# Performance work log

Hardware: AMD Instinct MI355X
Metric: run time of the kernel (lower is better)

Reference implementation:

```python
import jax, jax.numpy as jnp
import numpy as np
import math

NUM_CONVS = 4
GN_GROUPS = 32
GN_EPS = 1e-5
FPN_STRIDES = (8, 16, 32, 64, 128)
PRIOR_PROB = 0.01


def conv3x3(x, w, b):
    # x: [N,C,H,W], w: [O,I,3,3]
    y = jax.lax.conv_general_dilated(
        x, w, window_strides=(1, 1), padding='SAME',
        dimension_numbers=('NCHW', 'OIHW', 'NCHW'))
    return y + b[None, :, None, None]


def group_norm(x, gamma, beta):
    n, c, h, w = x.shape
    xg = x.reshape(n, GN_GROUPS, c // GN_GROUPS, h, w)
    mean = xg.mean(axis=(2, 3, 4), keepdims=True)
    var = xg.var(axis=(2, 3, 4), keepdims=True)
    xn = ((xg - mean) * jax.lax.rsqrt(var + GN_EPS)).reshape(n, c, h, w)
    return xn * gamma[None, :, None, None] + beta[None, :, None, None]


def subnet(x, ws, bs, gws, gbs):
    # NUM_CONVS x (conv3x3 -> GN -> ReLU)
    for i in range(NUM_CONVS):
        x = jax.nn.relu(group_norm(conv3x3(x, ws[i], bs[i]), gws[i], gbs[i]))
    return x


def permute_to_N_HWA_K(x, k):
    n = x.shape[0]
    return x.transpose(0, 2, 3, 1).reshape(n, -1, k)


def setup_inputs() -> dict:
    key = jax.random.key(0)
    ks = jax.random.split(key, 16)
    C, K = 256, 80
    feats = {
        'p3': jax.random.normal(ks[0], (1, C, 80, 80), jnp.float32),
        'p4': jax.random.normal(ks[1], (1, C, 40, 40), jnp.float32),
        'p5': jax.random.normal(ks[2], (1, C, 20, 20), jnp.float32),
        'p6': jax.random.normal(ks[3], (1, C, 10, 10), jnp.float32),
        'p7': jax.random.normal(ks[4], (1, C, 5, 5), jnp.float32),
    }
    std = 0.01
    bias_value = -math.log((1 - PRIOR_PROB) / PRIOR_PROB)
    params = {
        'cls_w': std * jax.random.normal(ks[5], (NUM_CONVS, C, C, 3, 3), jnp.float32),
        'cls_b': jnp.zeros((NUM_CONVS, C), jnp.float32),
        'cls_gn_w': jnp.ones((NUM_CONVS, C), jnp.float32),
        'cls_gn_b': jnp.zeros((NUM_CONVS, C), jnp.float32),
        'box_w': std * jax.random.normal(ks[6], (NUM_CONVS, C, C, 3, 3), jnp.float32),
        'box_b': jnp.zeros((NUM_CONVS, C), jnp.float32),
        'box_gn_w': jnp.ones((NUM_CONVS, C), jnp.float32),
        'box_gn_b': jnp.zeros((NUM_CONVS, C), jnp.float32),
        'score_w': std * jax.random.normal(ks[7], (K, C, 3, 3), jnp.float32),
        'score_b': jnp.full((K,), bias_value, jnp.float32),
        'pred_w': std * jax.random.normal(ks[8], (4, C, 3, 3), jnp.float32),
        'pred_b': jnp.zeros((4,), jnp.float32),
        'iou_w': std * jax.random.normal(ks[9], (1, C, 3, 3), jnp.float32),
        'iou_b': jnp.zeros((1,), jnp.float32),
        'scales': jnp.ones((5,), jnp.float32),
    }
    return {**feats, **params}


def reference(p3, p4, p5, p6, p7,
              cls_w, cls_b, cls_gn_w, cls_gn_b,
              box_w, box_b, box_gn_w, box_gn_b,
              score_w, score_b, pred_w, pred_b, iou_w, iou_b, scales):
    features = [p3, p4, p5, p6, p7]
    logits, bbox_reg, ious = [], [], []
    for l, feat in enumerate(features):
        c = subnet(feat, cls_w, cls_b, cls_gn_w, cls_gn_b)
        b = subnet(feat, box_w, box_b, box_gn_w, box_gn_b)
        logit = conv3x3(c, score_w, score_b)          # [N,80,H,W]
        iou = conv3x3(b, iou_w, iou_b)                # [N,1,H,W]
        bp = conv3x3(b, pred_w, pred_b) * scales[l]   # Scale module
        # norm_reg_targets=True branch
        reg = jax.nn.relu(bp) * FPN_STRIDES[l]        # [N,4,H,W]
        logits.append(permute_to_N_HWA_K(logit, 80))
        bbox_reg.append(permute_to_N_HWA_K(reg, 4))
        ious.append(permute_to_N_HWA_K(iou, 1))
    box_cls = jnp.concatenate(logits, axis=1)    # [N, sumHW, 80]
    box_delta = jnp.concatenate(bbox_reg, axis=1)  # [N, sumHW, 4]
    box_iou = jnp.concatenate(ious, axis=1)      # [N, sumHW, 1]
    # pack into one array for a single output: [N, sumHW, 85]
    return jnp.concatenate([box_cls, box_delta, box_iou], axis=-1)
```

## Files before the change

### kernel.cpp

```cpp
#include <hip/hip_runtime.h>

typedef unsigned short u16;
typedef __attribute__((ext_vector_type(8))) short bf16x8;
typedef __attribute__((ext_vector_type(4))) float f32x4;

#define NLEV 5
#define CCH 256
#define KTOT 2304
#define P_TOT 8525
#define PP_TOT 9165
#define PLS (PP_TOT*64)
#define HSTR 11776

__constant__ int   c_HW[NLEV]     = {6400, 1600, 400, 100, 25};
__constant__ int   c_W[NLEV]      = {80, 40, 20, 10, 5};
__constant__ int   c_off[NLEV]    = {0, 6400, 8000, 8400, 8500};
__constant__ int   c_poff[NLEV]   = {0, 6724, 8488, 8972, 9116};
__constant__ int   c_tls[NLEV+1]  = {0, 50, 65, 71, 73, 74};
__constant__ int   c_ntx[NLEV]    = {5, 3, 2, 1, 1};
__constant__ float c_stridef[NLEV]= {8.f, 16.f, 32.f, 64.f, 128.f};

__device__ __forceinline__ u16 f2bf(float f){
  union { float f; unsigned u; } v; v.f = f;
  unsigned r = v.u + 0x7fffu + ((v.u >> 16) & 1u);
  return (u16)(r >> 16);
}

__device__ __forceinline__ void g2l16(const u16* g, u16* l, int lane){
#if defined(__has_builtin)
#if __has_builtin(__builtin_amdgcn_global_load_lds)
  __builtin_amdgcn_global_load_lds(
      (const __attribute__((address_space(1))) unsigned int*)g,
      (__attribute__((address_space(3))) unsigned int*)l, 16, 0, 0);
  return;
#endif
#endif
  *(uint4*)(l + lane*8) = *(const uint4*)g;
}

#define WAIT_VM4   0x0F74
#define WAIT_VM10  0x0F7A
#define WAIT_VM0   0x0F70
#define WAIT_LGKM0 0xC07F

template<int MODE>
__global__ __launch_bounds__(256, 2) void gemm_conv(
    const u16* __restrict__ Xc, const u16* __restrict__ Xb,
    const u16* __restrict__ Wc, const u16* __restrict__ Wb,
    const float* __restrict__ bc, const float* __restrict__ bb,
    float* __restrict__ Yc, float* __restrict__ Yb,
    float* __restrict__ stats,
    const float* __restrict__ predb, const float* __restrict__ ioub,
    const float* __restrict__ scales, float* __restrict__ out)
{
  __shared__ u16 hB[2*HSTR];
  __shared__ u16 sA[4][2][2048];
  __shared__ float sstat[16][2];

  const int ptile = blockIdx.x;
  const int mtile = (MODE == 0) ? blockIdx.y : 0;
  const int br = blockIdx.z;
  int lv = 0;
  #pragma unroll
  for (int i = 1; i < NLEV; i++) if (ptile >= c_tls[i]) lv = i;
  const int tidx = ptile - c_tls[lv];
  const int ntx = c_ntx[lv];
  const int ty0 = (tidx / ntx) * 8, tx0 = (tidx - (tidx / ntx) * ntx) * 16;
  const int W = c_W[lv], wrow2 = W + 2;

  const int tid = threadIdx.x, wv = tid >> 6, ln = tid & 63;
  const int quad = ln >> 4, l15 = ln & 15;

  const u16* __restrict__ X  = br ? Xb : Xc;
  const u16* __restrict__ WA = br ? Wb : Wc;

  const int ASTR = (MODE == 0) ? 16384 : 8192;
  const u16* abase = WA +
      (size_t)(((MODE == 0) ? mtile*16 : 0) + wv*4) * 512 + ln*8;

  const u16* hptr[6]; int hslab[6];
  #pragma unroll
  for (int i = 0; i < 6; i++) {
    int j = wv + 4*i;
    if (j > 22) j -= 4;
    hslab[i] = j;
    const int item = j*64 + ln;
    int hp = item >> 3; if (hp >= 180) hp -= 180;
    const int g = item & 7;
    const int hy = hp / 18, hx = hp - hy*18;
    const int prow = c_poff[lv] + (ty0 + hy)*wrow2 + tx0 + hx;
    hptr[i] = X + (size_t)prow*64 + ((g ^ (hp & 7)) << 3);
  }

  auto stageH = [&](int plane) {
    u16* dst = &hB[(plane & 1) * HSTR];
    const size_t cof = (size_t)plane * PLS;
    #pragma unroll
    for (int i = 0; i < 6; i++)
      g2l16(hptr[i] + cof, dst + hslab[i]*512, ln);
  };
  auto stageA = [&](int s, int b) {
    const u16* as = abase + (size_t)s * ASTR;
    u16* da = &sA[wv][b][0];
    #pragma unroll
    for (int j = 0; j < 4; j++) g2l16(as + j*512, da + j*512, ln);
  };

  f32x4 acc[2][8];
  #pragma unroll
  for (int i = 0; i < 2; i++)
    #pragma unroll
    for (int j = 0; j < 8; j++) acc[i][j] = (f32x4){0.f, 0.f, 0.f, 0.f};

  if (MODE == 0 && tid < 32) sstat[tid >> 1][tid & 1] = 0.f;

  stageH(0);
  stageH(1);
  stageA(0, 0);
  stageA(4, 1);
  __syncthreads();

  int cc = 0, tap = 0;
  #pragma unroll 1
  for (int t = 0; t < 36; t++) {
    if (t == 10 || t == 19) __builtin_amdgcn_s_waitcnt(WAIT_VM10);
    else if (t == 35)       __builtin_amdgcn_s_waitcnt(WAIT_VM0);
    else                    __builtin_amdgcn_s_waitcnt(WAIT_VM4);
    if (tap == 0 && cc > 0) {
      __builtin_amdgcn_sched_barrier(0);
      __builtin_amdgcn_s_barrier();
      __builtin_amdgcn_sched_barrier(0);
      if (cc < 3) stageH(cc + 1);
    }
    const u16* myA = &sA[wv][t & 1][0];
    const u16* hpl = &hB[(cc & 1) * HSTR];
    const int dh = tap / 3, dw = tap - dh*3;
    bf16x8 af[2][2], bf[2][8];
    #pragma unroll
    for (int sub = 0; sub < 2; sub++) {
      const int q = sub*4 + quad;
      const int swzA = (q ^ (l15 & 7)) * 8;
      #pragma unroll
      for (int mt = 0; mt < 2; mt++)
        af[sub][mt] = *(const bf16x8*)&myA[(mt*16 + l15)*64 + swzA];
      #pragma unroll
      for (int nt = 0; nt < 8; nt++) {
        const int hp = (nt + dh)*18 + l15 + dw;
        bf[sub][nt] = *(const bf16x8*)&hpl[hp*64 + ((q ^ (hp & 7)) << 3)];
      }
    }
    __builtin_amdgcn_s_waitcnt(WAIT_LGKM0);
    if (t < 34) {
      int tap2 = tap + 2, cc2 = cc;
      if (tap2 >= 9) { tap2 -= 9; cc2++; }
      stageA(tap2*4 + cc2, t & 1);
    }
    #pragma unroll
    for (int sub = 0; sub < 2; sub++)
      #pragma unroll
      for (int mt = 0; mt < 2; mt++)
        #pragma unroll
        for (int nt = 0; nt < 8; nt++)
          acc[mt][nt] = __builtin_amdgcn_mfma_f32_16x16x32_bf16(
              af[sub][mt], bf[sub][nt], acc[mt][nt], 0, 0, 0);
    if (++tap == 9) { tap = 0; cc++; }
  }

  const int gx = tx0 + l15;
  if (MODE == 0) {
    const float* __restrict__ bias = br ? bb : bc;
    float* __restrict__ Y = br ? Yb : Yc;
    #pragma unroll
    for (int mt = 0; mt < 2; mt++) {
      const int mloc = wv*32 + mt*16 + quad*4;
      const int mrow = mtile*128 + mloc;
      const f32x4 bv = *(const f32x4*)&bias[mrow];
      float s = 0.f, sq = 0.f;
      #pragma unroll
      for (int nt = 0; nt < 8; nt++) {
        const int gy = ty0 + nt;
        f32x4 v = acc[mt][nt] + bv;
        if (gy < W && gx < W) {
          const size_t n = (size_t)(c_off[lv] + gy*W + gx);
          *(f32x4*)&Y[n*CCH + mrow] = v;
          #pragma unroll
          for (int r = 0; r < 4; r++) { s += v[r]; sq += v[r]*v[r]; }
        }
      }
      #pragma unroll
      for (int o = 1; o < 16; o <<= 1) { s += __shfl_xor(s, o); sq += __shfl_xor(sq, o); }
      if (l15 == 0) {
        const int g = mloc >> 3;
        atomicAdd(&sstat[g][0], s);
        atomicAdd(&sstat[g][1], sq);
      }
    }
    __syncthreads();
    if (tid < 32) {
      const int g = tid >> 1, c = tid & 1;
      atomicAdd(&stats[((br*NLEV + lv)*32 + mtile*16 + g)*2 + c], sstat[g][c]);
    }
  } else {
    const float scl = scales[lv];
    const float stf = c_stridef[lv];
    #pragma unroll
    for (int mt = 0; mt < 2; mt++) {
      const int mr0 = wv*32 + mt*16 + quad*4;
      if (mr0 >= 85) continue;
      #pragma unroll
      for (int nt = 0; nt < 8; nt++) {
        const int gy = ty0 + nt;
        if (gy >= W || gx >= W) continue;
        const size_t n = (size_t)(c_off[lv] + gy*W + gx);
        const f32x4 v = acc[mt][nt];
        #pragma unroll
        for (int r = 0; r < 4; r++) {
          const int m = mr0 + r;
          if (br == 0) {
            if (m < 80) out[n*85 + m] = v[r] + bc[m];
          } else {
            if (m < 4) {
              const float t = (v[r] + predb[m]) * scl;
              out[n*85 + 80 + m] = fmaxf(t, 0.f) * stf;
            } else if (m == 4) {
              out[n*85 + 84] = v[r] + ioub[0];
            }
          }
        }
      }
    }
  }
}

__global__ __launch_bounds__(256) void gn_relu(
    const float* __restrict__ Yc, const float* __restrict__ Yb,
    const float* __restrict__ stats,
    const float* __restrict__ gwc, const float* __restrict__ gbc,
    const float* __restrict__ gwb, const float* __restrict__ gbb,
    u16* __restrict__ Xc, u16* __restrict__ Xb)
{
  const int t = blockIdx.x * 256 + threadIdx.x;
  if (t >= 2 * P_TOT * 32) return;
  const int br = t / (P_TOT * 32);
  const int r  = t - br * (P_TOT * 32);
  const int pg = r >> 5;
  const int c0 = (r & 31) << 3;
  int lv = 0;
  #pragma unroll
  for (int i = 1; i < NLEV; i++) if (pg >= c_off[i]) lv = i;
  const int pl = pg - c_off[lv];
  const int Wl = c_W[lv];
  const int g = c0 >> 3;
  const float* st = &stats[(((size_t)br*NLEV + lv)*32 + g)*2];
  const float cnt = 8.f * (float)c_HW[lv];
  const float mean = st[0] / cnt;
  const float var  = st[1] / cnt - mean*mean;
  const float rstd = rsqrtf(var + 1e-5f);
  const float* Y  = br ? Yb : Yc;
  const float* gw = br ? gwb : gwc;
  const float* gb = br ? gbb : gbc;
  u16* X = br ? Xb : Xc;
  const float* y = &Y[(size_t)pg*CCH + c0];
  const int h = pl / Wl, wi = pl - h*Wl;
  const size_t pidx = (size_t)(c_poff[lv] + (h+1)*(Wl+2) + (wi+1));
  union { u16 u[8]; uint4 v; } pk;
  #pragma unroll
  for (int i = 0; i < 8; i++) {
    const float v = (y[i] - mean)*rstd*gw[c0+i] + gb[c0+i];
    pk.u[i] = f2bf(fmaxf(v, 0.f));
  }
  *(uint4*)&X[(size_t)(c0 >> 6)*PLS + pidx*64 + (c0 & 63)] = pk.v;
}

__global__ __launch_bounds__(256) void feat2bf(
    const float* __restrict__ p3, const float* __restrict__ p4,
    const float* __restrict__ p5, const float* __restrict__ p6,
    const float* __restrict__ p7, u16* __restrict__ X)
{
  const int t = blockIdx.x * 256 + threadIdx.x;
  if (t >= P_TOT * 32) return;
  const int pg = t >> 5, c0 = (t & 31) << 3;
  int lv = 0;
  #pragma unroll
  for (int i = 1; i < NLEV; i++) if (pg >= c_off[i]) lv = i;
  const int pl = pg - c_off[lv];
  const float* src = lv==0 ? p3 : lv==1 ? p4 : lv==2 ? p5 : lv==3 ? p6 : p7;
  const int HW = c_HW[lv], Wl = c_W[lv];
  const int h = pl / Wl, wi = pl - h*Wl;
  const size_t pidx = (size_t)(c_poff[lv] + (h+1)*(Wl+2) + (wi+1));
  union { u16 u[8]; uint4 v; } pk;
  #pragma unroll
  for (int i = 0; i < 8; i++)
    pk.u[i] = f2bf(src[(size_t)(c0+i)*HW + pl]);
  *(uint4*)&X[(size_t)(c0 >> 6)*PLS + pidx*64 + (c0 & 63)] = pk.v;
}

__global__ __launch_bounds__(256) void wconv(
    const float* __restrict__ cw, const float* __restrict__ bw,
    u16* __restrict__ Wc, u16* __restrict__ Wb)
{
  const size_t N = (size_t)4*256*KTOT;
  const size_t t = (size_t)blockIdx.x * 256 + threadIdx.x;
  if (t >= 2*N) return;
  const float* src = (t < N) ? cw : bw;
  u16* dst = (t < N) ? Wc : Wb;
  const size_t i = (t < N) ? t : t - N;
  const size_t lc = i / KTOT;
  const int kk = (int)(i - lc*KTOT);
  const int l = (int)(lc >> 8), co = (int)(lc & 255);
  const int tap = kk >> 8, ci = kk & 255;
  const int s = kk >> 6, kl = kk & 63;
  const int r = co & 7, p = (kl >> 3) ^ r;
  const size_t d = (size_t)l*589824 +
      ((size_t)((s*32 + (co >> 3))*64 + r*8 + p))*8 + (kl & 7);
  dst[d] = f2bf(src[(lc*256 + ci)*9 + tap]);
}

__global__ __launch_bounds__(256) void hconv(
    const float* __restrict__ sw, const float* __restrict__ pw,
    const float* __restrict__ iw, u16* __restrict__ Whc, u16* __restrict__ Whb)
{
  const int N = 128 * KTOT;
  const int t = blockIdx.x * 256 + threadIdx.x;
  if (t >= 2*N) return;
  const int i = (t < N) ? t : t - N;
  const int co = i / KTOT, kk = i - co*KTOT;
  const int tap = kk >> 8, ci = kk & 255;
  const int s = kk >> 6, kl = kk & 63;
  const int r = co & 7, p = (kl >> 3) ^ r;
  const size_t d = ((size_t)((s*16 + (co >> 3))*64 + r*8 + p))*8 + (kl & 7);
  float v = 0.f;
  if (t < N) {
    if (co < 80) v = sw[(co*256 + ci)*9 + tap];
    Whc[d] = f2bf(v);
  } else {
    if (co < 4)       v = pw[(co*256 + ci)*9 + tap];
    else if (co == 4) v = iw[ci*9 + tap];
    Whb[d] = f2bf(v);
  }
}

extern "C" void kernel_launch(void* const* d_in, const int* in_sizes, int n_in,
                              void* d_out, int out_size, void* d_ws, size_t ws_size,
                              hipStream_t stream)
{
  const float* p3      = (const float*)d_in[0];
  const float* p4      = (const float*)d_in[1];
  const float* p5      = (const float*)d_in[2];
  const float* p6      = (const float*)d_in[3];
  const float* p7      = (const float*)d_in[4];
  const float* cls_w   = (const float*)d_in[5];
  const float* cls_b   = (const float*)d_in[6];
  const float* cls_gw  = (const float*)d_in[7];
  const float* cls_gb  = (const float*)d_in[8];
  const float* box_w   = (const float*)d_in[9];
  const float* box_b   = (const float*)d_in[10];
  const float* box_gw  = (const float*)d_in[11];
  const float* box_gb  = (const float*)d_in[12];
  const float* score_w = (const float*)d_in[13];
  const float* score_b = (const float*)d_in[14];
  const float* pred_w  = (const float*)d_in[15];
  const float* pred_b  = (const float*)d_in[16];
  const float* iou_w   = (const float*)d_in[17];
  const float* iou_b   = (const float*)d_in[18];
  const float* scales  = (const float*)d_in[19];
  float* out = (float*)d_out;

  char* w = (char*)d_ws;
  size_t o = 0;
  auto alloc = [&](size_t b) { void* p = w + o; o += (b + 255) & ~(size_t)255; return p; };
  u16*   XF = (u16*)alloc((size_t)PP_TOT*CCH*2);
  u16*   XC = (u16*)alloc((size_t)PP_TOT*CCH*2);
  u16*   XB = (u16*)alloc((size_t)PP_TOT*CCH*2);
  float* ST = (float*)alloc((size_t)4*2*NLEV*32*2*4);
  u16*  WRC = (u16*)alloc((size_t)4*256*KTOT*2);
  u16*  WRB = (u16*)alloc((size_t)4*256*KTOT*2);
  u16*  WHC = (u16*)alloc((size_t)128*KTOT*2);
  u16*  WHB = (u16*)alloc((size_t)128*KTOT*2);
  float* YC = (float*)alloc((size_t)P_TOT*CCH*4);
  float* YB = (float*)alloc((size_t)P_TOT*CCH*4);

  hipMemsetAsync(XF, 0, (size_t)3*PP_TOT*CCH*2 + (size_t)4*2*NLEV*32*2*4, stream);

  wconv<<<dim3((unsigned)(((size_t)2*4*256*KTOT + 255)/256)), 256, 0, stream>>>(cls_w, box_w, WRC, WRB);
  hconv<<<dim3((2*128*KTOT + 255)/256), 256, 0, stream>>>(score_w, pred_w, iou_w, WHC, WHB);
  feat2bf<<<dim3((P_TOT*32 + 255)/256), 256, 0, stream>>>(p3, p4, p5, p6, p7, XF);

  const u16* xci = XF; const u16* xbi = XF;
  for (int l = 0; l < 4; l++) {
    float* STl = ST + (size_t)l*2*NLEV*32*2;
    gemm_conv<0><<<dim3(74, 2, 2), 256, 0, stream>>>(
        xci, xbi, WRC + (size_t)l*589824, WRB + (size_t)l*589824,
        cls_b + l*256, box_b + l*256, YC, YB, STl,
        nullptr, nullptr, nullptr, nullptr);
    gn_relu<<<dim3((2*P_TOT*32 + 255)/256), 256, 0, stream>>>(
        YC, YB, STl, cls_gw + l*256, cls_gb + l*256, box_gw + l*256, box_gb + l*256,
        XC, XB);
    xci = XC; xbi = XB;
  }
  gemm_conv<1><<<dim3(74, 1, 2), 256, 0, stream>>>(
      xci, xbi, WHC, WHB, score_b, nullptr, nullptr, nullptr, nullptr,
      pred_b, iou_b, scales, out);
}
```

Measured before the change: 358.3 us.

## Software-pipeline LDS fragment reads across iterations and raise MFMA priority

The main conv GEMM loop now splits each step's two K sub-slices so that LDS reads for the second half and for the next iteration's first half overlap the MFMAs of the current half, using partial lgkmcnt waits. Register double-buffering replaces the read-all-then-compute structure, and the H-slab and A-weight staging and vmcnt waits are rescheduled around the channel-chunk barriers. MFMA blocks are wrapped in s_setprio to favour matrix issue. The cost targeted is LDS read latency exposed before the MFMA burst; the price is more live registers and intricate wait-count bookkeeping that could break correctness if miscounted.

```diff
diff --git a/kernel.cpp b/kernel.cpp
--- a/kernel.cpp
+++ b/kernel.cpp
@@ -38,10 +38,11 @@
   *(uint4*)(l + lane*8) = *(const uint4*)g;
 }
 
-#define WAIT_VM4   0x0F74
-#define WAIT_VM10  0x0F7A
-#define WAIT_VM0   0x0F70
-#define WAIT_LGKM0 0xC07F
+#define WAIT_VM4    0x0F74
+#define WAIT_VM10   0x0F7A
+#define WAIT_VM0    0x0F70
+#define WAIT_LGKM0  0xC07F
+#define WAIT_LGKM10 0xCA7F
 
 template<int MODE>
 __global__ __launch_bounds__(256, 2) void gemm_conv(
@@ -112,6 +113,44 @@
     #pragma unroll
     for (int j = 0; j < 8; j++) acc[i][j] = (f32x4){0.f, 0.f, 0.f, 0.f};
 
+  bf16x8 af0[2], bf0[8], af1[2], bf1[8];
+
+  auto rdA = [&](const u16* myA, int q, bf16x8 (&af)[2]) {
+    const int swzA = (q ^ (l15 & 7)) * 8;
+    #pragma unroll
+    for (int mt = 0; mt < 2; mt++)
+      af[mt] = *(const bf16x8*)&myA[(mt*16 + l15)*64 + swzA];
+  };
+  auto rdB = [&](const u16* hpl, int q, int tapv, bf16x8 (&bf)[8]) {
+    const int dh = tapv / 3, dw = tapv - dh*3;
+    #pragma unroll
+    for (int nt = 0; nt < 8; nt++) {
+      const int hp = (nt + dh)*18 + l15 + dw;
+      bf[nt] = *(const bf16x8*)&hpl[hp*64 + ((q ^ (hp & 7)) << 3)];
+    }
+  };
+  auto mm = [&](const bf16x8 (&af)[2], const bf16x8 (&bf)[8]) {
+    __builtin_amdgcn_s_setprio(1);
+    #pragma unroll
+    for (int mt = 0; mt < 2; mt++)
+      #pragma unroll
+      for (int nt = 0; nt < 8; nt++)
+        acc[mt][nt] = __builtin_amdgcn_mfma_f32_16x16x32_bf16(
+            af[mt], bf[nt], acc[mt][nt], 0, 0, 0);
+    __builtin_amdgcn_s_setprio(0);
+  };
+  auto stageAfor = [&](int t_, int tap_, int cc_) {
+    int tap2 = tap_ + 2, cc2 = cc_;
+    if (tap2 >= 9) { tap2 -= 9; cc2++; }
+    stageA(tap2*4 + cc2, t_ & 1);
+  };
+  auto pre = [&](int t_, int tap_, int cc_) {
+    int tapn = tap_ + 1, ccn = cc_;
+    if (tapn >= 9) { tapn = 0; ccn++; }
+    rdA(&sA[wv][(t_ + 1) & 1][0], quad, af0);
+    rdB(&hB[(ccn & 1) * HSTR], quad, tapn, bf0);
+  };
+
   if (MODE == 0 && tid < 32) sstat[tid >> 1][tid & 1] = 0.f;
 
   stageH(0);
@@ -119,50 +158,52 @@
   stageA(0, 0);
   stageA(4, 1);
   __syncthreads();
+  rdA(&sA[wv][0][0], quad, af0);
+  rdB(&hB[0], quad, 0, bf0);
 
   int cc = 0, tap = 0;
   #pragma unroll 1
   for (int t = 0; t < 36; t++) {
-    if (t == 10 || t == 19) __builtin_amdgcn_s_waitcnt(WAIT_VM10);
-    else if (t == 35)       __builtin_amdgcn_s_waitcnt(WAIT_VM0);
-    else                    __builtin_amdgcn_s_waitcnt(WAIT_VM4);
+    const u16* myA = &sA[wv][t & 1][0];
+    const u16* hpl = &hB[(cc & 1) * HSTR];
     if (tap == 0 && cc > 0) {
       __builtin_amdgcn_sched_barrier(0);
       __builtin_amdgcn_s_barrier();
       __builtin_amdgcn_sched_barrier(0);
-      if (cc < 3) stageH(cc + 1);
-    }
-    const u16* myA = &sA[wv][t & 1][0];
-    const u16* hpl = &hB[(cc & 1) * HSTR];
-    const int dh = tap / 3, dw = tap - dh*3;
-    bf16x8 af[2][2], bf[2][8];
-    #pragma unroll
-    for (int sub = 0; sub < 2; sub++) {
-      const int q = sub*4 + quad;
-      const int swzA = (q ^ (l15 & 7)) * 8;
-      #pragma unroll
-      for (int mt = 0; mt < 2; mt++)
-        af[sub][mt] = *(const bf16x8*)&myA[(mt*16 + l15)*64 + swzA];
-      #pragma unroll
-      for (int nt = 0; nt < 8; nt++) {
-        const int hp = (nt + dh)*18 + l15 + dw;
-        bf[sub][nt] = *(const bf16x8*)&hpl[hp*64 + ((q ^ (hp & 7)) << 3)];
+    }
+    if (t == 18 || t == 27) {
+      __builtin_amdgcn_s_waitcnt(WAIT_VM4);
+      rdA(myA, quad, af0);       rdB(hpl, quad,     tap, bf0);
+      rdA(myA, 4 + quad, af1);   rdB(hpl, 4 + quad, tap, bf1);
+      __builtin_amdgcn_s_waitcnt(WAIT_LGKM10);
+      mm(af0, bf0);
+      __builtin_amdgcn_s_waitcnt(WAIT_LGKM0);
+      stageAfor(t, tap, cc);
+      if (t == 18) stageH(3);
+      if (t == 18) __builtin_amdgcn_s_waitcnt(WAIT_VM10);
+      else         __builtin_amdgcn_s_waitcnt(WAIT_VM4);
+      pre(t, tap, cc);
+      __builtin_amdgcn_sched_barrier(0);
+      mm(af1, bf1);
+    } else {
+      rdA(myA, 4 + quad, af1);
+      rdB(hpl, 4 + quad, tap, bf1);
+      __builtin_amdgcn_s_waitcnt(WAIT_LGKM10);
+      mm(af0, bf0);
+      __builtin_amdgcn_s_waitcnt(WAIT_LGKM0);
+      if (t < 34) stageAfor(t, tap, cc);
+      if (t == 9) stageH(2);
+      if (t < 35 && t != 17 && t != 26) {
+        if (t == 9 || t == 10 || t == 19)
+             __builtin_amdgcn_s_waitcnt(WAIT_VM10);
+        else if (t == 34)
+             __builtin_amdgcn_s_waitcnt(WAIT_VM0);
+        else __builtin_amdgcn_s_waitcnt(WAIT_VM4);
+        pre(t, tap, cc);
       }
-    }
-    __builtin_amdgcn_s_waitcnt(WAIT_LGKM0);
-    if (t < 34) {
-      int tap2 = tap + 2, cc2 = cc;
-      if (tap2 >= 9) { tap2 -= 9; cc2++; }
-      stageA(tap2*4 + cc2, t & 1);
-    }
-    #pragma unroll
-    for (int sub = 0; sub < 2; sub++)
-      #pragma unroll
-      for (int mt = 0; mt < 2; mt++)
-        #pragma unroll
-        for (int nt = 0; nt < 8; nt++)
-          acc[mt][nt] = __builtin_amdgcn_mfma_f32_16x16x32_bf16(
-              af[sub][mt], bf[sub][nt], acc[mt][nt], 0, 0, 0);
+      __builtin_amdgcn_sched_barrier(0);
+      mm(af1, bf1);
+    }
     if (++tap == 9) { tap = 0; cc++; }
   }
 
```

Result: slower. 426.6 us (+19.1%).

## Load weight fragments directly to registers and reuse halo B rows across kernel rows

Applied to the files above, without the earlier changes.

Weight (A) fragments now load straight from global memory into registers in an MFMA-fragment-ordered layout, produced by rewritten wconv/hconv packing. This removes the LDS staging buffer for weights and its double-buffer waits. The loop now iterates over the three kernel columns and loads ten halo rows of B once per column, reusing them across all three kernel rows (dh). That cuts LDS reads per MFMA but holds about 12 A fragments in registers, which raises register pressure and exposes global-load latency that only the loop structure hides.

```diff
diff --git a/kernel.cpp b/kernel.cpp
--- a/kernel.cpp
+++ b/kernel.cpp
@@ -38,10 +38,7 @@
   *(uint4*)(l + lane*8) = *(const uint4*)g;
 }
 
-#define WAIT_VM4   0x0F74
-#define WAIT_VM10  0x0F7A
-#define WAIT_VM0   0x0F70
-#define WAIT_LGKM0 0xC07F
+#define WAIT_VM12  0x0F7C
 
 template<int MODE>
 __global__ __launch_bounds__(256, 2) void gemm_conv(
@@ -54,7 +51,6 @@
     const float* __restrict__ scales, float* __restrict__ out)
 {
   __shared__ u16 hB[2*HSTR];
-  __shared__ u16 sA[4][2][2048];
   __shared__ float sstat[16][2];
 
   const int ptile = blockIdx.x;
@@ -74,9 +70,9 @@
   const u16* __restrict__ X  = br ? Xb : Xc;
   const u16* __restrict__ WA = br ? Wb : Wc;
 
-  const int ASTR = (MODE == 0) ? 16384 : 8192;
-  const u16* abase = WA +
-      (size_t)(((MODE == 0) ? mtile*16 : 0) + wv*4) * 512 + ln*8;
+  const int SZ = (MODE == 0) ? 16384 : 8192;
+  const u16* aln = WA +
+      (size_t)((((MODE == 0) ? (mtile*4 + wv) : wv)) * 2048 + quad*128 + l15*8);
 
   const u16* hptr[6]; int hslab[6];
   #pragma unroll
@@ -99,71 +95,66 @@
     for (int i = 0; i < 6; i++)
       g2l16(hptr[i] + cof, dst + hslab[i]*512, ln);
   };
-  auto stageA = [&](int s, int b) {
-    const u16* as = abase + (size_t)s * ASTR;
-    u16* da = &sA[wv][b][0];
-    #pragma unroll
-    for (int j = 0; j < 4; j++) g2l16(as + j*512, da + j*512, ln);
+
+  f32x4 acc[2][8];
+  #pragma unroll
+  for (int i = 0; i < 2; i++)
+    #pragma unroll
+    for (int j = 0; j < 8; j++) acc[i][j] = (f32x4){0.f, 0.f, 0.f, 0.f};
+
+  bf16x8 af[3][2][2];
+  auto loadA = [&](int cc_, int dw_) {
+    #pragma unroll
+    for (int dh = 0; dh < 3; dh++) {
+      const u16* p = aln + (size_t)((dh*3 + dw_)*4 + cc_) * SZ;
+      #pragma unroll
+      for (int sub = 0; sub < 2; sub++)
+        #pragma unroll
+        for (int mt = 0; mt < 2; mt++)
+          af[dh][sub][mt] = *(const bf16x8*)(p + sub*1024 + mt*512);
+    }
   };
-
-  f32x4 acc[2][8];
-  #pragma unroll
-  for (int i = 0; i < 2; i++)
-    #pragma unroll
-    for (int j = 0; j < 8; j++) acc[i][j] = (f32x4){0.f, 0.f, 0.f, 0.f};
 
   if (MODE == 0 && tid < 32) sstat[tid >> 1][tid & 1] = 0.f;
 
   stageH(0);
   stageH(1);
-  stageA(0, 0);
-  stageA(4, 1);
+  loadA(0, 0);
   __syncthreads();
 
-  int cc = 0, tap = 0;
+  int cc = 0, dw = 0;
   #pragma unroll 1
-  for (int t = 0; t < 36; t++) {
-    if (t == 10 || t == 19) __builtin_amdgcn_s_waitcnt(WAIT_VM10);
-    else if (t == 35)       __builtin_amdgcn_s_waitcnt(WAIT_VM0);
-    else                    __builtin_amdgcn_s_waitcnt(WAIT_VM4);
-    if (tap == 0 && cc > 0) {
+  for (int u = 0; u < 12; u++) {
+    if (dw == 0 && cc > 0) {
+      __builtin_amdgcn_s_waitcnt(WAIT_VM12);
       __builtin_amdgcn_sched_barrier(0);
       __builtin_amdgcn_s_barrier();
       __builtin_amdgcn_sched_barrier(0);
       if (cc < 3) stageH(cc + 1);
     }
-    const u16* myA = &sA[wv][t & 1][0];
     const u16* hpl = &hB[(cc & 1) * HSTR];
-    const int dh = tap / 3, dw = tap - dh*3;
-    bf16x8 af[2][2], bf[2][8];
     #pragma unroll
     for (int sub = 0; sub < 2; sub++) {
       const int q = sub*4 + quad;
-      const int swzA = (q ^ (l15 & 7)) * 8;
-      #pragma unroll
-      for (int mt = 0; mt < 2; mt++)
-        af[sub][mt] = *(const bf16x8*)&myA[(mt*16 + l15)*64 + swzA];
-      #pragma unroll
-      for (int nt = 0; nt < 8; nt++) {
-        const int hp = (nt + dh)*18 + l15 + dw;
-        bf[sub][nt] = *(const bf16x8*)&hpl[hp*64 + ((q ^ (hp & 7)) << 3)];
+      bf16x8 bf[10];
+      #pragma unroll
+      for (int n2 = 0; n2 < 10; n2++) {
+        const int hp = n2*18 + l15 + dw;
+        bf[n2] = *(const bf16x8*)&hpl[hp*64 + ((q ^ (hp & 7)) << 3)];
       }
-    }
-    __builtin_amdgcn_s_waitcnt(WAIT_LGKM0);
-    if (t < 34) {
-      int tap2 = tap + 2, cc2 = cc;
-      if (tap2 >= 9) { tap2 -= 9; cc2++; }
-      stageA(tap2*4 + cc2, t & 1);
-    }
-    #pragma unroll
-    for (int sub = 0; sub < 2; sub++)
-      #pragma unroll
-      for (int mt = 0; mt < 2; mt++)
+      #pragma unroll
+      for (int dh = 0; dh < 3; dh++)
         #pragma unroll
-        for (int nt = 0; nt < 8; nt++)
-          acc[mt][nt] = __builtin_amdgcn_mfma_f32_16x16x32_bf16(
-              af[sub][mt], bf[sub][nt], acc[mt][nt], 0, 0, 0);
-    if (++tap == 9) { tap = 0; cc++; }
+        for (int mt = 0; mt < 2; mt++)
+          #pragma unroll
+          for (int nt = 0; nt < 8; nt++)
+            acc[mt][nt] = __builtin_amdgcn_mfma_f32_16x16x32_bf16(
+                af[dh][sub][mt], bf[nt + dh], acc[mt][nt], 0, 0, 0);
+    }
+    int dwn = dw + 1, ccn = cc;
+    if (dwn == 3) { dwn = 0; ccn++; }
+    if (u < 11) loadA(ccn, dwn);
+    dw = dwn; cc = ccn;
   }
 
   const int gx = tx0 + l15;
@@ -310,9 +301,9 @@
   const int l = (int)(lc >> 8), co = (int)(lc & 255);
   const int tap = kk >> 8, ci = kk & 255;
   const int s = kk >> 6, kl = kk & 63;
-  const int r = co & 7, p = (kl >> 3) ^ r;
-  const size_t d = (size_t)l*589824 +
-      ((size_t)((s*32 + (co >> 3))*64 + r*8 + p))*8 + (kl & 7);
+  const size_t d = (size_t)l*589824 + (size_t)s*16384 +
+      (size_t)((co >> 5)*2048 + (kl >> 5)*1024 + ((co >> 4) & 1)*512 +
+               ((kl >> 3) & 3)*128 + (co & 15)*8 + (kl & 7));
   dst[d] = f2bf(src[(lc*256 + ci)*9 + tap]);
 }
 
@@ -327,8 +318,9 @@
   const int co = i / KTOT, kk = i - co*KTOT;
   const int tap = kk >> 8, ci = kk & 255;
   const int s = kk >> 6, kl = kk & 63;
-  const int r = co & 7, p = (kl >> 3) ^ r;
-  const size_t d = ((size_t)((s*16 + (co >> 3))*64 + r*8 + p))*8 + (kl & 7);
+  const size_t d = (size_t)s*8192 +
+      (size_t)((co >> 5)*2048 + (kl >> 5)*1024 + ((co >> 4) & 1)*512 +
+               ((kl >> 3) & 3)*128 + (co & 15)*8 + (kl & 7));
   float v = 0.f;
   if (t < N) {
     if (co < 80) v = sw[(co*256 + ci)*9 + tap];
```

Result: faster. 329.0 us (-8.2%).
